# Optimization experiments

Hardware: AMD Instinct MI355X
Metric: run time of the kernel (lower is better)

## Reference

```python
import jax, jax.numpy as jnp
import numpy as np
from math import sqrt

NUM_HEADS = 8
HIDDEN = 768
ATTN_DIM = HIDDEN // NUM_HEADS  # 96
NEG = -1e10


def setup_inputs() -> dict:
    key = jax.random.key(0)
    ks = jax.random.split(key, 6)
    b, s, dim = 8, 1024, 768
    scale = 1.0 / sqrt(dim)
    return {
        "span_embeddings": jax.random.normal(ks[0], (b, s, dim), dtype=jnp.float32),
        "span_tags": jax.random.randint(ks[1], (b, s), 0, 5),
        "w_weight": jax.random.normal(ks[2], (1, dim), dtype=jnp.float32) * scale,
        "w_q": jax.random.normal(ks[3], (HIDDEN, dim), dtype=jnp.float32) * scale,
        "w_k": jax.random.normal(ks[4], (HIDDEN, dim), dtype=jnp.float32) * scale,
        "w_v": jax.random.normal(ks[5], (HIDDEN, dim), dtype=jnp.float32) * scale,
    }


def reference(span_embeddings, span_tags, w_weight, w_q, w_k, w_v):
    b, s, _ = span_embeddings.shape
    pad = span_tags == 0  # [b, s]

    # additive span attention weights: Linear(dim -> 1), mask padded, softmax over seq
    attn_weights = span_embeddings @ w_weight.T  # [b, s, 1]
    attn_weights = jnp.where(pad[:, :, None], NEG, attn_weights)
    attn_weights = jax.nn.softmax(attn_weights, axis=1)

    # NOTE: original views hidden as (attn_dim, num_heads) in that order
    qs = (span_embeddings @ w_q.T).reshape(b, s, ATTN_DIM, NUM_HEADS)
    ks = (span_embeddings @ w_k.T).reshape(b, s, ATTN_DIM, NUM_HEADS)
    vs = (span_embeddings @ w_v.T).reshape(b, s, ATTN_DIM, NUM_HEADS)

    rel = jnp.einsum('bqdh,bkdh->bqkh', qs, ks) / sqrt(ATTN_DIM)  # [b,q,k,h]
    # original masks along query axis (relevance_weights[span_tags.eq(0)] = NEG)
    rel = jnp.where(pad[:, :, None, None], NEG, rel)
    # original softmax(dim=-1) -> over the HEADS axis (faithful quirk)
    rel = jax.nn.softmax(rel, axis=-1)

    span_value = jnp.einsum('bqkh,bkdh->bqdh', rel, vs).reshape(b, s, HIDDEN)
    weighted_value = jnp.sum(attn_weights * span_value, axis=1)  # [b, hidden]
    return weighted_value
```

## Files before the change

### kernel.cpp

```cpp
#include <hip/hip_runtime.h>
#include <hip/hip_bf16.h>
#include <math.h>

#define NEGV (-1e10f)

typedef __attribute__((ext_vector_type(8))) short bf16x8;
typedef __attribute__((ext_vector_type(4))) float f32x4;
typedef __attribute__((ext_vector_type(16))) float f32x16;

static __device__ __forceinline__ unsigned short f2bf(float f) {
  unsigned int u = __builtin_bit_cast(unsigned int, f);
  unsigned int r = (u + 0x7fffu + ((u >> 16) & 1u)) >> 16;
  return (unsigned short)r;
}
static __device__ __forceinline__ float bf2f(unsigned short v) {
  return __builtin_bit_cast(float, (unsigned int)v << 16);
}

#define GLD16(g, l)                                                   \
  __builtin_amdgcn_global_load_lds(                                   \
      (const __attribute__((address_space(1))) void*)(g),             \
      (__attribute__((address_space(3))) void*)(l), 16, 0, 0)

__global__ __launch_bounds__(256) void cast_inputs(
    const float* __restrict__ emb, const int* __restrict__ tags,
    const float* __restrict__ ww, const float* __restrict__ wq,
    const float* __restrict__ wk, const float* __restrict__ wv,
    unsigned short* __restrict__ embbf, float* __restrict__ logits,
    unsigned short* __restrict__ wbf) {
  int bx = blockIdx.x;
  if (bx < 2048) {
    int w = threadIdx.x >> 6, lane = threadIdx.x & 63;
    int row = bx * 4 + w;
    const float4* src = (const float4*)(emb + (size_t)row * 768);
    const float4* wsrc = (const float4*)ww;
    ushort4* dst = (ushort4*)(embbf + (size_t)row * 768);
    float d = 0.f;
#pragma unroll
    for (int j = 0; j < 3; j++) {
      int idx = lane + 64 * j;
      float4 v = src[idx];
      float4 wv = wsrc[idx];
      d += v.x * wv.x + v.y * wv.y + v.z * wv.z + v.w * wv.w;
      ushort4 o;
      o.x = f2bf(v.x); o.y = f2bf(v.y); o.z = f2bf(v.z); o.w = f2bf(v.w);
      dst[idx] = o;
    }
#pragma unroll
    for (int off = 32; off; off >>= 1) d += __shfl_xor(d, off);
    if (lane == 0) logits[row] = (tags[row] == 0) ? NEGV : d;
  } else {
    int g = bx - 2048;
    int z = g / 576;
    int idx = (g - z * 576) * 256 + threadIdx.x;
    const float* src = (z == 0) ? wq : (z == 1) ? wk : wv;
    float4 v = ((const float4*)src)[idx];
    ushort4 o;
    o.x = f2bf(v.x); o.y = f2bf(v.y); o.z = f2bf(v.z); o.w = f2bf(v.w);
    if (z == 2) {
      ((ushort4*)(wbf + (size_t)z * 589824))[idx] = o;
    } else {
      int f = idx / 192;
      int col4 = idx - f * 192;
      int h = f & 7, dg = f >> 3;
      int tt = dg >> 4, ddl = dg & 15;
      int wn = ddl >> 3, cb = (ddl >> 2) & 1, j = ddl & 3;
      int orow = tt * 128 + wn * 64 + j * 16 + cb * 8 + h;
      ((ushort4*)(wbf + (size_t)z * 589824))[orow * 192 + col4] = o;
    }
  }
}

__global__ __launch_bounds__(256) void softmax_aw(
    const float* __restrict__ logits, float* __restrict__ aw) {
  __shared__ float red[4];
  int b = blockIdx.x, t = threadIdx.x;
  const float* L = logits + b * 1024;
  float x0 = L[t], x1 = L[t + 256], x2 = L[t + 512], x3 = L[t + 768];
  float m = fmaxf(fmaxf(x0, x1), fmaxf(x2, x3));
#pragma unroll
  for (int off = 32; off; off >>= 1) m = fmaxf(m, __shfl_xor(m, off));
  if ((t & 63) == 0) red[t >> 6] = m;
  __syncthreads();
  m = fmaxf(fmaxf(red[0], red[1]), fmaxf(red[2], red[3]));
  float e0 = __expf(x0 - m), e1 = __expf(x1 - m), e2 = __expf(x2 - m),
        e3 = __expf(x3 - m);
  float s = e0 + e1 + e2 + e3;
#pragma unroll
  for (int off = 32; off; off >>= 1) s += __shfl_xor(s, off);
  __syncthreads();
  if ((t & 63) == 0) red[t >> 6] = s;
  __syncthreads();
  float inv = 1.0f / (red[0] + red[1] + red[2] + red[3]);
  float* A = aw + b * 1024;
  A[t] = e0 * inv; A[t + 256] = e1 * inv;
  A[t + 512] = e2 * inv; A[t + 768] = e3 * inv;
}

__global__ __launch_bounds__(256) void qkv_gemm(
    const unsigned short* __restrict__ A, const unsigned short* __restrict__ Wbf,
    unsigned short* __restrict__ Qf, unsigned short* __restrict__ Kf,
    unsigned short* __restrict__ Vbf) {
  __shared__ __align__(16) unsigned short sm[17408];
  unsigned short* As = sm;
  unsigned short* Bs = sm + 8192;
  int z = blockIdx.z;
  const unsigned short* B = Wbf + (size_t)z * 589824;
  int mb = blockIdx.x * 128, nb = blockIdx.y * 128;
  int tid = threadIdx.x;
  int w = tid >> 6, lane = tid & 63;
  int wm = w >> 1, wn = w & 1;
  int c = lane & 15, quad = lane >> 4;
  int lrow = lane >> 2;
  int lcol = ((lane & 3) ^ (lrow & 3)) * 8;
  const unsigned short* Ag = A + (size_t)(mb + w * 32 + lrow) * 768 + lcol;
  const unsigned short* Bg = B + (size_t)(nb + w * 32 + lrow) * 768 + lcol;
  int woff = w * 1024;

#define PREFETCH(buf, kb)                                              \
  do {                                                                 \
    GLD16(Ag + (kb), As + (buf) * 4096 + woff);                        \
    GLD16(Ag + (kb) + 16 * 768, As + (buf) * 4096 + woff + 512);       \
    GLD16(Bg + (kb), Bs + (buf) * 4096 + woff);                        \
    GLD16(Bg + (kb) + 16 * 768, Bs + (buf) * 4096 + woff + 512);       \
  } while (0)

  f32x4 acc[4][4];
#pragma unroll
  for (int i = 0; i < 4; i++)
#pragma unroll
    for (int j = 0; j < 4; j++) acc[i][j] = 0;

  PREFETCH(0, 0);
  for (int it = 0; it < 24; it++) {
    __syncthreads();
    if (it + 1 < 24) PREFETCH((it + 1) & 1, (it + 1) * 32);
    const unsigned short* Ab = As + (it & 1) * 4096;
    const unsigned short* Bb = Bs + (it & 1) * 4096;
    int sw = (quad ^ (c & 3)) * 8;
    bf16x8 af[4], bfr[4];
#pragma unroll
    for (int i = 0; i < 4; i++)
      af[i] = *(const bf16x8*)&Ab[(wm * 64 + i * 16 + c) * 32 + sw];
#pragma unroll
    for (int j = 0; j < 4; j++)
      bfr[j] = *(const bf16x8*)&Bb[(wn * 64 + j * 16 + c) * 32 + sw];
#pragma unroll
    for (int i = 0; i < 4; i++)
#pragma unroll
      for (int j = 0; j < 4; j++)
        acc[i][j] = __builtin_amdgcn_mfma_f32_16x16x32_bf16(af[i], bfr[j],
                                                            acc[i][j], 0, 0, 0);
  }
  __syncthreads();

  if (z == 2) {
#pragma unroll
    for (int i = 0; i < 4; i++)
#pragma unroll
      for (int j = 0; j < 4; j++)
#pragma unroll
        for (int r = 0; r < 4; r++) {
          int rl = wm * 64 + i * 16 + quad * 4 + r;
          int cl = wn * 64 + j * 16 + c;
          sm[rl * 136 + cl] = f2bf(acc[i][j][r]);
        }
    __syncthreads();
#pragma unroll
    for (int it2 = 0; it2 < 8; it2++) {
      int g2 = it2 * 256 + tid;
      int rl = g2 >> 4;
      int cu = (g2 & 15) * 8;
      bf16x8 vdat = *(const bf16x8*)&sm[rl * 136 + cu];
      *(bf16x8*)&Vbf[(size_t)(mb + rl) * 768 + nb + cu] = vdat;
    }
  } else {
    unsigned short* O = (z == 0) ? Qf : Kf;
#pragma unroll
    for (int i = 0; i < 4; i++) {
#pragma unroll
      for (int r = 0; r < 4; r++) {
        int qlr = wm * 64 + i * 16 + quad * 4 + r;
        int chunkL = (qlr >> 5) * 8 + (c & 7);
        int lane32 = (qlr & 31) + wn * 32;
        ushort4 pk;
        pk.x = f2bf(acc[i][0][r]);
        pk.y = f2bf(acc[i][1][r]);
        pk.z = f2bf(acc[i][2][r]);
        pk.w = f2bf(acc[i][3][r]);
        *(ushort4*)&sm[chunkL * 520 + lane32 * 8 + 4 * (c >> 3)] = pk;
      }
    }
    __syncthreads();
    int bq = mb >> 10;
    int qt32g0 = (mb & 1023) >> 5;
    int tt = blockIdx.y;
#pragma unroll
    for (int it2 = 0; it2 < 8; it2++) {
      int g = it2 * 256 + tid;
      int chunkL = g >> 6;
      int off = (g & 63) * 8;
      bf16x8 vdat = *(const bf16x8*)&sm[chunkL * 520 + off];
      int qt32 = qt32g0 + (chunkL >> 3), h = chunkL & 7;
      size_t dst = ((((size_t)(bq * 32 + qt32) * 8 + h) * 6 + tt) << 9) + off;
      *(bf16x8*)&O[dst] = vdat;
    }
  }
#undef PREFETCH
}

__global__ __launch_bounds__(512) void attn(
    const unsigned short* __restrict__ Qf, const unsigned short* __restrict__ Kf,
    const float* __restrict__ aw, float* __restrict__ Ptp) {
  __shared__ __align__(16) unsigned short Qs[49152];
  __shared__ float pbuf[2048];
  int b = blockIdx.z, qb = blockIdx.y, kb = blockIdx.x;
  int tid = threadIdx.x, w = tid >> 6, lane = tid & 63;
  int wq2 = w >> 2, wk2 = w & 3;

#pragma unroll
  for (int call = 0; call < 12; call++) {
    int cc = call * 8 + w;
    int q32 = cc / 48, rem = cc - q32 * 48;
    size_t src =
        ((size_t)((b * 32 + qb * 2 + q32) * 48 + rem) << 9) + (size_t)lane * 8;
    GLD16(Qf + src, Qs + cc * 512);
  }
  __syncthreads();

  const unsigned short* Kc =
      Kf + ((size_t)(b * 32 + kb * 4 + wk2) * 48 << 9) + (size_t)lane * 8;
  const unsigned short* Qw = Qs + wq2 * 48 * 512 + (size_t)lane * 8;

  f32x16 acc[8];
#pragma unroll
  for (int h = 0; h < 8; h++) acc[h] = 0;
#pragma unroll
  for (int h = 0; h < 8; h++) {
#pragma unroll
    for (int t = 0; t < 6; t++) {
      bf16x8 a = *(const bf16x8*)(Qw + (size_t)(h * 6 + t) * 512);
      bf16x8 bb = *(const bf16x8*)(Kc + (size_t)(h * 6 + t) * 512);
      acc[h] = __builtin_amdgcn_mfma_f32_32x32x16_bf16(a, bb, acc[h], 0, 0, 0);
    }
  }

  float awv[16];
#pragma unroll
  for (int reg = 0; reg < 16; reg++) {
    int row = (reg & 3) + 8 * (reg >> 2) + 4 * (lane >> 5);
    awv[reg] = aw[b * 1024 + qb * 64 + wq2 * 32 + row];
  }
  float partial[8];
#pragma unroll
  for (int h = 0; h < 8; h++) partial[h] = 0.f;
  const float C2 = 0.10206207261596577f * 1.4426950408889634f;
#pragma unroll
  for (int reg = 0; reg < 16; reg++) {
    float v[8];
    float ssum = 0.f;
#pragma unroll
    for (int h = 0; h < 8; h++) {
      float e = exp2f(acc[h][reg] * C2);
      v[h] = e;
      ssum += e;
    }
    float g = awv[reg] * __builtin_amdgcn_rcpf(ssum);
#pragma unroll
    for (int h = 0; h < 8; h++) partial[h] += v[h] * g;
  }
#pragma unroll
  for (int h = 0; h < 8; h++) {
    float v = partial[h];
    v += __shfl_xor(v, 32);
    partial[h] = v;
  }
  if (lane < 32) {
#pragma unroll
    for (int h = 0; h < 8; h++) pbuf[w * 256 + lane * 8 + h] = partial[h];
  }
  __syncthreads();
#pragma unroll
  for (int half = 0; half < 2; half++) {
    int idx = half * 512 + tid;
    int wko = idx >> 8, rem2 = idx & 255;
    float s = pbuf[wko * 256 + rem2] + pbuf[(wko + 4) * 256 + rem2];
    int kcol = rem2 >> 3, h = rem2 & 7;
    Ptp[(((size_t)qb * 8 + b) * 1024 + kb * 128 + wko * 32 + kcol) * 8 + h] = s;
  }
}

__global__ __launch_bounds__(256) void finalize(
    const float* __restrict__ Ptp, const unsigned short* __restrict__ Vbf,
    float* __restrict__ out) {
  __shared__ float ps[256];
  int kc = blockIdx.x, b = blockIdx.y;
  int t = threadIdx.x;
  {
    int k = kc * 32 + (t >> 3), h = t & 7;
    float s = 0.f;
#pragma unroll
    for (int qc = 0; qc < 16; qc++)
      s += Ptp[(((size_t)qc * 8 + b) * 1024 + k) * 8 + h];
    ps[t] = s;
  }
  __syncthreads();
  if (t < 192) {
    int o0 = t * 4;
    int hb = o0 & 7;
    float a0 = 0, a1 = 0, a2 = 0, a3 = 0;
    const unsigned short* Vb = Vbf + ((size_t)b * 1024 + kc * 32) * 768 + o0;
#pragma unroll 4
    for (int kk = 0; kk < 32; kk++) {
      ushort4 vv = *(const ushort4*)(Vb + (size_t)kk * 768);
      const float* p = &ps[kk * 8 + hb];
      a0 += p[0] * bf2f(vv.x);
      a1 += p[1] * bf2f(vv.y);
      a2 += p[2] * bf2f(vv.z);
      a3 += p[3] * bf2f(vv.w);
    }
    atomicAdd(&out[b * 768 + o0], a0);
    atomicAdd(&out[b * 768 + o0 + 1], a1);
    atomicAdd(&out[b * 768 + o0 + 2], a2);
    atomicAdd(&out[b * 768 + o0 + 3], a3);
  }
}

extern "C" void kernel_launch(void* const* d_in, const int* in_sizes, int n_in,
                              void* d_out, int out_size, void* d_ws,
                              size_t ws_size, hipStream_t stream) {
  const float* emb = (const float*)d_in[0];
  const int* tags = (const int*)d_in[1];
  const float* ww = (const float*)d_in[2];
  const float* wq = (const float*)d_in[3];
  const float* wk = (const float*)d_in[4];
  const float* wv = (const float*)d_in[5];
  float* out = (float*)d_out;
  char* ws = (char*)d_ws;
  unsigned short* embbf = (unsigned short*)(ws + 0);
  unsigned short* wbf   = (unsigned short*)(ws + 12582912);
  unsigned short* Qf    = (unsigned short*)(ws + 16121856);
  unsigned short* Kf    = (unsigned short*)(ws + 28704768);
  unsigned short* Vbf   = (unsigned short*)(ws + 41287680);
  float* logits         = (float*)(ws + 53870592);
  float* aw             = (float*)(ws + 53903360);
  float* Ptp            = (float*)(ws + 53936128);

  hipMemsetAsync(out, 0, 8 * 768 * sizeof(float), stream);
  cast_inputs<<<3776, 256, 0, stream>>>(emb, tags, ww, wq, wk, wv, embbf,
                                        logits, wbf);
  softmax_aw<<<8, 256, 0, stream>>>(logits, aw);
  qkv_gemm<<<dim3(64, 6, 3), 256, 0, stream>>>(embbf, wbf, Qf, Kf, Vbf);
  attn<<<dim3(8, 16, 8), 512, 0, stream>>>(Qf, Kf, aw, Ptp);
  finalize<<<dim3(32, 8), 256, 0, stream>>>(Ptp, Vbf, out);
}
```

Measured before the change: 186.7 us.

## Shrink attn tiles to 64x64, drop LDS Q staging, remap grid batch-fastest

The attn kernel now uses 256-thread blocks covering a 64x64 query-key tile instead of 512 threads on 64x128. Q is read directly from global memory rather than staged through a 96KB LDS buffer, which removes the LDS footprint and the sync before compute. The grid is flattened to 2048 blocks with batch as the fastest index, giving more blocks and likely better occupancy. The cost is less Q reuse across waves, so Q and K traffic rises and depends more on L2 hits.

```diff
diff --git a/kernel.cpp b/kernel.cpp
--- a/kernel.cpp
+++ b/kernel.cpp
@@ -209,28 +209,18 @@
 #undef PREFETCH
 }
 
-__global__ __launch_bounds__(512) void attn(
+__global__ __launch_bounds__(256) void attn(
     const unsigned short* __restrict__ Qf, const unsigned short* __restrict__ Kf,
     const float* __restrict__ aw, float* __restrict__ Ptp) {
-  __shared__ __align__(16) unsigned short Qs[49152];
-  __shared__ float pbuf[2048];
-  int b = blockIdx.z, qb = blockIdx.y, kb = blockIdx.x;
+  __shared__ float pbuf[1024];
+  int id = blockIdx.x;
+  int b = id & 7, qb = (id >> 3) & 15, kb = id >> 7;
   int tid = threadIdx.x, w = tid >> 6, lane = tid & 63;
-  int wq2 = w >> 2, wk2 = w & 3;
-
-#pragma unroll
-  for (int call = 0; call < 12; call++) {
-    int cc = call * 8 + w;
-    int q32 = cc / 48, rem = cc - q32 * 48;
-    size_t src =
-        ((size_t)((b * 32 + qb * 2 + q32) * 48 + rem) << 9) + (size_t)lane * 8;
-    GLD16(Qf + src, Qs + cc * 512);
-  }
-  __syncthreads();
-
-  const unsigned short* Kc =
-      Kf + ((size_t)(b * 32 + kb * 4 + wk2) * 48 << 9) + (size_t)lane * 8;
-  const unsigned short* Qw = Qs + wq2 * 48 * 512 + (size_t)lane * 8;
+  int wq = w >> 1, wk = w & 1;
+  const unsigned short* Qb =
+      Qf + ((size_t)(b * 32 + qb * 2 + wq) * 48) * 512 + (size_t)lane * 8;
+  const unsigned short* Kb =
+      Kf + ((size_t)(b * 32 + kb * 2 + wk) * 48) * 512 + (size_t)lane * 8;
 
   f32x16 acc[8];
 #pragma unroll
@@ -239,8 +229,8 @@
   for (int h = 0; h < 8; h++) {
 #pragma unroll
     for (int t = 0; t < 6; t++) {
-      bf16x8 a = *(const bf16x8*)(Qw + (size_t)(h * 6 + t) * 512);
-      bf16x8 bb = *(const bf16x8*)(Kc + (size_t)(h * 6 + t) * 512);
+      bf16x8 a = *(const bf16x8*)(Qb + (size_t)(h * 6 + t) * 512);
+      bf16x8 bb = *(const bf16x8*)(Kb + (size_t)(h * 6 + t) * 512);
       acc[h] = __builtin_amdgcn_mfma_f32_32x32x16_bf16(a, bb, acc[h], 0, 0, 0);
     }
   }
@@ -249,7 +239,7 @@
 #pragma unroll
   for (int reg = 0; reg < 16; reg++) {
     int row = (reg & 3) + 8 * (reg >> 2) + 4 * (lane >> 5);
-    awv[reg] = aw[b * 1024 + qb * 64 + wq2 * 32 + row];
+    awv[reg] = aw[b * 1024 + qb * 64 + wq * 32 + row];
   }
   float partial[8];
 #pragma unroll
@@ -281,12 +271,10 @@
   }
   __syncthreads();
 #pragma unroll
-  for (int half = 0; half < 2; half++) {
-    int idx = half * 512 + tid;
-    int wko = idx >> 8, rem2 = idx & 255;
-    float s = pbuf[wko * 256 + rem2] + pbuf[(wko + 4) * 256 + rem2];
-    int kcol = rem2 >> 3, h = rem2 & 7;
-    Ptp[(((size_t)qb * 8 + b) * 1024 + kb * 128 + wko * 32 + kcol) * 8 + h] = s;
+  for (int wk2 = 0; wk2 < 2; wk2++) {
+    float s = pbuf[wk2 * 256 + tid] + pbuf[(2 + wk2) * 256 + tid];
+    int kcol = tid >> 3, h = tid & 7;
+    Ptp[(((size_t)qb * 8 + b) * 1024 + kb * 64 + wk2 * 32 + kcol) * 8 + h] = s;
   }
 }
 
@@ -351,6 +339,6 @@
                                         logits, wbf);
   softmax_aw<<<8, 256, 0, stream>>>(logits, aw);
   qkv_gemm<<<dim3(64, 6, 3), 256, 0, stream>>>(embbf, wbf, Qf, Kf, Vbf);
-  attn<<<dim3(8, 16, 8), 512, 0, stream>>>(Qf, Kf, aw, Ptp);
+  attn<<<2048, 256, 0, stream>>>(Qf, Kf, aw, Ptp);
   finalize<<<dim3(32, 8), 256, 0, stream>>>(Ptp, Vbf, out);
 }
```

After: 171.1 us. 8.4% less time.
